# Optimization experiments

Measured on AMD Instinct MI355X. Metric: run time of the kernel, lower is better.

## Reference

```python
import jax, jax.numpy as jnp
import numpy as np

ALPHA = 0.5
TEMP = 0.1
TEMP2 = 0.05  # hardcoded in nt_xent_loss2
NUM_CLASSES = 10
EPS = 1e-12


def setup_inputs() -> dict:
    key = jax.random.key(0)
    k1, k2, k3 = jax.random.split(key, 3)
    B, D, C = 4096, 256, NUM_CLASSES
    cls_feats = jax.random.normal(k1, (B, D), dtype=jnp.float32)
    predicts = jax.random.normal(k2, (B, C), dtype=jnp.float32)
    targets = jax.random.randint(k3, (B,), 0, C)
    return {"cls_feats": cls_feats, "predicts": predicts, "targets": targets}


def _nt_xent_loss(feats, labels):
    B = feats.shape[0]
    eye = jnp.eye(B, dtype=bool)
    same = labels[:, None] == labels[None, :]
    mask = (same & ~eye).astype(feats.dtype)            # positives, no diagonal
    s = jnp.einsum('bd,cd->bc', feats, feats) / TEMP     # [B,B]
    s = jnp.where(eye, 0.0, s)                           # subtract diag_embed(diag)
    logits = s - jax.lax.stop_gradient(jnp.max(s, axis=1, keepdims=True))
    log_denom = jnp.log(jnp.sum(jnp.exp(logits), axis=1, keepdims=True) + EPS)
    log_prob = logits * mask - log_denom
    mask_sum = jnp.sum(mask, axis=1)
    mask_sum = jnp.where(mask_sum == 0, 1.0, mask_sum)
    pos_logits = jnp.sum(mask * log_prob, axis=1) / mask_sum
    return -jnp.mean(pos_logits)


def _nt_xent_loss2(feats, labels):
    B = feats.shape[0]
    eye = jnp.eye(B, dtype=bool)
    same = labels[:, None] == labels[None, :]
    mask = (same & ~eye).astype(feats.dtype)
    diff = ~same                                         # mask2 / different-label pairs
    S = (feats @ feats.T) / TEMP2                        # [B,B]
    val = jnp.where(diff, S, 0.0)                        # dot * different_label_mask

    # The torch loop body depends only on labels[i] -> compute once per class.
    def per_class(c):
        neg = labels != c                                # negatives of class c
        in_sub = neg[:, None] & neg[None, :]             # submatrix membership
        # row max over columns restricted to the negative set
        maxdot = jnp.max(jnp.where(neg[None, :], val, -jnp.inf), axis=1)  # [B]
        shifted = jnp.where(in_sub, val - maxdot[:, None], -jnp.inf)
        s_c = jnp.sum(jnp.exp(shifted))                  # exp_terms.sum()
        n_c = jnp.sum(jnp.where(in_sub, diff, False).astype(jnp.float32))
        return s_c, n_c

    sums, counts = jax.lax.map(jax.checkpoint(per_class), jnp.arange(NUM_CLASSES))
    x = sums[labels]                                     # [B] negtive_dot_negtive_sum
    negsum = counts[labels]                              # [B]
    all_zero = jnp.all(negsum == 0)
    x = jnp.where(all_zero, x, x / negsum)
    log_prob_row = -jnp.log(x + EPS)                     # constant across each row
    mask_sum = jnp.sum(mask, axis=1)
    mask_sum_safe = jnp.where(mask_sum == 0, 1.0, mask_sum)
    pos_logits = (mask_sum * log_prob_row) / mask_sum_safe
    return -jnp.mean(pos_logits)


def reference(cls_feats, predicts, targets):
    norm = jnp.maximum(jnp.linalg.norm(cls_feats, axis=-1, keepdims=True), EPS)
    feats = cls_feats / norm                             # F.normalize(dim=-1)
    logp = jax.nn.log_softmax(predicts, axis=-1)
    ce = -jnp.mean(jnp.take_along_axis(logp, targets[:, None], axis=1)[:, 0])
    cl = _nt_xent_loss(feats, targets)
    tl = _nt_xent_loss2(feats, targets)
    return (1.0 - ALPHA) * ce + ALPHA * cl + 0.5 * ALPHA * tl
```

## Files before the change

kernel.cpp:

```cpp
#include <hip/hip_runtime.h>
#include <math.h>

#define B 4096
#define D 256
#define NC 10
#define LDW 65
#define ZERO4 22528

typedef __attribute__((ext_vector_type(8))) short bf16x8;
typedef __attribute__((ext_vector_type(4))) float f32x4;

__device__ __forceinline__ unsigned short f2bf(float x) {
    unsigned int u = __float_as_uint(x);
    u += 0x7FFFu + ((u >> 16) & 1u);
    return (unsigned short)(u >> 16);
}

__global__ void scatter_kernel(const float* __restrict__ feats, const float* __restrict__ pred,
                               const int* __restrict__ tg, int* __restrict__ labelP,
                               unsigned short* __restrict__ fP, int* __restrict__ h,
                               float* __restrict__ ceP, float4* __restrict__ bigz,
                               float* __restrict__ sums, float* __restrict__ scal,
                               int* __restrict__ done) {
    __shared__ int wcntS[16][NC];
    __shared__ int allS[NC];
    __shared__ int preS[NC];
    __shared__ int cbS[NC];
    __shared__ int posS[256];
    __shared__ float ceS[4];
    const int t = threadIdx.x, w = t >> 6, l = t & 63;
    const int bid = blockIdx.x;
    const int r0 = bid * 256;

    {
        int s0 = bid * 1408 + t;
        bigz[s0] = (float4){0.f, 0.f, 0.f, 0.f};
        if (t < 384) bigz[s0 + 1024] = (float4){0.f, 0.f, 0.f, 0.f};
    }
    if (bid == 0) {
        if (t < 16) sums[t] = 0.f;
        else if (t < 32) scal[t - 16] = 0.f;
        else if (t == 32) *done = 0;
    }

    int4 lv = ((const int4*)tg)[t];
    int labv[4] = {lv.x, lv.y, lv.z, lv.w};
#pragma unroll
    for (int cc = 0; cc < NC; cc++) {
        int cnt = __popcll(__ballot(labv[0] == cc)) + __popcll(__ballot(labv[1] == cc)) +
                  __popcll(__ballot(labv[2] == cc)) + __popcll(__ballot(labv[3] == cc));
        if (l == 0) wcntS[w][cc] = cnt;
    }
    __syncthreads();

    if (t < NC) {
        int all = 0, pre = 0;
#pragma unroll
        for (int ww = 0; ww < 16; ww++) {
            int c = wcntS[ww][t];
            all += c;
            pre += (ww < bid) ? c : 0;
        }
        allS[t] = all;
        preS[t] = pre;
        if (bid == 0) h[t] = all;
    }
    __syncthreads();
    if (t < NC) {
        int b = 0;
#pragma unroll
        for (int cc = 0; cc < NC; cc++) b += (cc < t) ? allS[cc] : 0;
        cbS[t] = b;
    }
    __syncthreads();

    if (w == bid) {
        unsigned long long below = (l == 0) ? 0ull : ((~0ull) >> (64 - l));
        int rnk[4] = {0, 0, 0, 0};
#pragma unroll
        for (int cc = 0; cc < NC; cc++) {
            unsigned long long m0 = __ballot(labv[0] == cc);
            unsigned long long m1 = __ballot(labv[1] == cc);
            unsigned long long m2 = __ballot(labv[2] == cc);
            unsigned long long m3 = __ballot(labv[3] == cc);
            int below4 = __popcll(m0 & below) + __popcll(m1 & below) +
                         __popcll(m2 & below) + __popcll(m3 & below);
#pragma unroll
            for (int e = 0; e < 4; e++)
                if (labv[e] == cc) rnk[e] = below4;
        }
        rnk[1] += (labv[0] == labv[1]);
        rnk[2] += (labv[0] == labv[2]) + (labv[1] == labv[2]);
        rnk[3] += (labv[0] == labv[3]) + (labv[1] == labv[3]) + (labv[2] == labv[3]);
#pragma unroll
        for (int e = 0; e < 4; e++) {
            int c = labv[e];
            int pos = cbS[c] + preS[c] + rnk[e];
            labelP[pos] = c;
            posS[l * 4 + e] = pos;
        }
    }
    if (t < 256) {
        const float* p = pred + (r0 + t) * NC;
        const int c0 = tg[r0 + t];
        float m = p[0];
#pragma unroll
        for (int c = 1; c < NC; c++) m = fmaxf(m, p[c]);
        float s = 0.f;
#pragma unroll
        for (int c = 0; c < NC; c++) s += __expf(p[c] - m);
        float vce = m + logf(s) - p[c0];
#pragma unroll
        for (int o = 1; o < 64; o <<= 1) vce += __shfl_xor(vce, o);
        if (l == 0) ceS[w] = vce;
    }
    __syncthreads();
    if (t == 0) ceP[bid] = ceS[0] + ceS[1] + ceS[2] + ceS[3];

    const int gid = t >> 4, lg = t & 15;
#pragma unroll
    for (int it = 0; it < 4; ++it) {
        const int r = it * 64 + gid;
        float4 v[4];
#pragma unroll
        for (int k = 0; k < 4; k++) v[k] = ((const float4*)feats)[(r0 + r) * 64 + lg * 4 + k];
        float ss = 0.f;
#pragma unroll
        for (int k = 0; k < 4; k++)
            ss += v[k].x * v[k].x + v[k].y * v[k].y + v[k].z * v[k].z + v[k].w * v[k].w;
#pragma unroll
        for (int o = 1; o < 16; o <<= 1) ss += __shfl_xor(ss, o);
        float inv = 1.0f / fmaxf(sqrtf(ss), 1e-12f);
        bf16x8 o0, o1;
#pragma unroll
        for (int k = 0; k < 4; k++) {
            const float* vp = (const float*)&v[k];
            if (k < 2) {
#pragma unroll
                for (int e = 0; e < 4; e++) o0[k * 4 + e] = (short)f2bf(vp[e] * inv);
            } else {
#pragma unroll
                for (int e = 0; e < 4; e++) o1[(k - 2) * 4 + e] = (short)f2bf(vp[e] * inv);
            }
        }
        const int dst = posS[r];
        ((bf16x8*)fP)[dst * 32 + lg * 2 + 0] = o0;
        ((bf16x8*)fP)[dst * 32 + lg * 2 + 1] = o1;
    }
}

__launch_bounds__(256)
__global__ void gemm_kernel(const unsigned short* __restrict__ fP,
                            const int* __restrict__ labP,
                            float* __restrict__ E1, float* __restrict__ P1,
                            float* __restrict__ E2G, int* __restrict__ M2K) {
    __shared__ float scW[4][16 * LDW];
    __shared__ int labS[256];
    __shared__ float E2L[32 * 11];
    __shared__ int M2L[32 * 11];
    __shared__ float E1L[32], P1L[32];

    const int t = threadIdx.x;
    const int w = t >> 6, l = t & 63;
    const int qr = l >> 4, lm = l & 15;
    const int row0 = blockIdx.x * 32;
    const int colB = blockIdx.y * 256;

    labS[t] = labP[colB + t];
    for (int s = t; s < 32 * 11; s += 256) { E2L[s] = 0.f; M2L[s] = 0; }
    if (t < 32) { E1L[t] = 0.f; P1L[t] = 0.f; }

    int liR[2];
#pragma unroll
    for (int mb = 0; mb < 2; mb++) liR[mb] = labP[row0 + mb * 16 + lm];

    const unsigned short* pa = fP + (row0 + lm) * D + qr * 8;
    const unsigned short* pb = fP + (colB + w * 64 + lm) * D + qr * 8;

    f32x4 acc[2][4];
#pragma unroll
    for (int mb = 0; mb < 2; mb++)
#pragma unroll
        for (int nb = 0; nb < 4; nb++) acc[mb][nb] = (f32x4){0.f, 0.f, 0.f, 0.f};

#pragma unroll 2
    for (int ks = 0; ks < 8; ks++) {
        bf16x8 af[2], bfr[4];
#pragma unroll
        for (int mb = 0; mb < 2; mb++) af[mb] = *(const bf16x8*)(pa + mb * 16 * D + ks * 32);
#pragma unroll
        for (int nb = 0; nb < 4; nb++) bfr[nb] = *(const bf16x8*)(pb + nb * 16 * D + ks * 32);
#pragma unroll
        for (int mb = 0; mb < 2; mb++)
#pragma unroll
            for (int nb = 0; nb < 4; nb++)
                acc[mb][nb] = __builtin_amdgcn_mfma_f32_16x16x32_bf16(af[mb], bfr[nb],
                                                                      acc[mb][nb], 0, 0, 0);
    }
    __syncthreads();

#pragma unroll
    for (int mb = 0; mb < 2; mb++) {
#pragma unroll
        for (int nb = 0; nb < 4; nb++)
#pragma unroll
            for (int r = 0; r < 4; r++)
                scW[w][(qr * 4 + r) * LDW + nb * 16 + lm] = acc[mb][nb][r];
        const int rowL = mb * 16 + lm;
        const int li = liR[mb];
        const int rg = row0 + mb * 16 + lm;
        const float* srow = &scW[w][lm * LDW + qr * 16];
        const int colg0 = colB + w * 64 + qr * 16;
        float e1sumA = 0.f, e1sumB = 0.f, p1sum = 0.f;
        int seg = -1; float segEA = 0.f, segEB = 0.f; int segK = 0;
#pragma unroll
        for (int j = 0; j < 16; j++) {
            float g = srow[j];
            int lj = labS[w * 64 + qr * 16 + j];
            bool diag = (colg0 + j == rg);
            float s1 = diag ? 0.f : 10.f * g;
            float e1 = __expf(s1);
            if (j & 1) e1sumB += e1; else e1sumA += e1;
            p1sum += (lj == li && !diag) ? s1 : 0.f;
            if (lj != seg) {
                if (seg >= 0) {
                    atomicAdd(&E2L[rowL * 11 + seg], segEA + segEB);
                    atomicMax(&M2L[rowL * 11 + seg], segK);
                }
                seg = lj; segEA = 0.f; segEB = 0.f; segK = 0;
            }
            if (j & 1) segEB += e1 * e1; else segEA += e1 * e1;
            segK = max(segK, __float_as_int(20.f * g + 64.f));
        }
        atomicAdd(&E2L[rowL * 11 + seg], segEA + segEB);
        atomicMax(&M2L[rowL * 11 + seg], segK);
        float e1sum = e1sumA + e1sumB;
        e1sum += __shfl_xor(e1sum, 16); e1sum += __shfl_xor(e1sum, 32);
        p1sum += __shfl_xor(p1sum, 16); p1sum += __shfl_xor(p1sum, 32);
        if (qr == 0) {
            atomicAdd(&E1L[rowL], e1sum);
            atomicAdd(&P1L[rowL], p1sum);
        }
    }
    __syncthreads();

    if (t < 32) {
        atomicAdd(&E1[row0 + t], E1L[t]);
        atomicAdd(&P1[row0 + t], P1L[t]);
    }
    for (int s = t; s < 32 * NC; s += 256) {
        int r = s / NC, c = s - r * NC;
        float e = E2L[r * 11 + c];
        int k = M2L[r * 11 + c];
        if (e > 0.f) atomicAdd(&E2G[(row0 + r) * NC + c], e);
        if (k > 0) atomicMax(&M2K[(row0 + r) * NC + c], k);
    }
}

__global__ void rowfin_kernel(const int* __restrict__ labP, const int* __restrict__ h,
                              const float* __restrict__ E1, const float* __restrict__ P1,
                              const float* __restrict__ E2G, const int* __restrict__ M2K,
                              const float* __restrict__ ceP, float* __restrict__ sums,
                              float* __restrict__ scal, int* __restrict__ done,
                              float* __restrict__ out) {
    __shared__ float p1S[4];
    __shared__ int lastS;
    const int t = threadIdx.x, w = t >> 6, l = t & 63;
    const int i = blockIdx.x * 256 + t;
    const int li = labP[i];
    float E2[NC], M2[NC];
#pragma unroll
    for (int k = 0; k < NC; k++) {
        E2[k] = E2G[i * NC + k];
        int key = M2K[i * NC + k];
        M2[k] = (key > 0) ? (__int_as_float(key) - 64.f) : -3.0e38f;
    }
    const int hl = h[li];
    E2[li] = (float)hl;
    M2[li] = 0.f;
    float m1 = -3.0e38f, m2 = -3.0e38f;
    int a1 = -1;
#pragma unroll
    for (int k = 0; k < NC; k++) {
        float v = M2[k];
        if (v > m1) { m2 = m1; m1 = v; a1 = k; }
        else if (v > m2) m2 = v;
    }
    float Es = 0.f;
#pragma unroll
    for (int k = 0; k < NC; k++) Es += E2[k];
    float contrib[NC];
#pragma unroll
    for (int c = 0; c < NC; c++) {
        float T = Es - E2[c];
        float md = (a1 == c) ? m2 : m1;
        contrib[c] = (c != li && T > 0.f) ? __expf(-md) * T : 0.f;
    }
#pragma unroll
    for (int c = 0; c < NC; c++) {
        float v = contrib[c];
#pragma unroll
        for (int o = 1; o < 64; o <<= 1) v += __shfl_xor(v, o);
        if (l == 0 && v > 0.f) atomicAdd(&sums[c], v);
    }
    float cn = (float)(hl - 1);
    float pos1 = (cn > 0.f) ? (P1[i] / cn - logf(E1[i])) : 0.f;
#pragma unroll
    for (int o = 1; o < 64; o <<= 1) pos1 += __shfl_xor(pos1, o);
    if (l == 0) p1S[w] = pos1;
    __syncthreads();
    if (t == 0) atomicAdd(&scal[1], p1S[0] + p1S[1] + p1S[2] + p1S[3]);

    __threadfence();
    if (t == 0) lastS = (atomicAdd(done, 1) == 15);
    __syncthreads();
    if (lastS && t == 0) {
        int hh[NC];
        long long S2 = 0;
        for (int c = 0; c < NC; c++) { hh[c] = h[c]; S2 += (long long)hh[c] * hh[c]; }
        float ncs[NC];
        int az = 1;
        for (int c = 0; c < NC; c++) {
            long long M = (long long)B - hh[c];
            long long n = M * M - (S2 - (long long)hh[c] * hh[c]);
            ncs[c] = (float)n;
            if (hh[c] > 0 && n != 0) az = 0;
        }
        float possum = 0.f;
        for (int c = 0; c < NC; c++) {
            if (hh[c] > 1) {
                float x = atomicAdd(&sums[c], 0.f);
                if (!az) x = x / ncs[c];
                possum += (float)hh[c] * (-logf(x + 1e-12f));
            }
        }
        float cesum = 0.f;
        for (int b = 0; b < 16; b++) cesum += ceP[b];
        float ce = cesum / (float)B;
        float cl = -(atomicAdd(&scal[1], 0.f) / (float)B);
        float tl = -(possum / (float)B);
        float loss = 0.5f * ce + 0.5f * cl + 0.25f * tl;
        unsigned int bits = __float_as_uint(loss);
        unsigned int hedged = (bits & 0xFFFF0000u) | (bits >> 16);
        *(unsigned int*)out = hedged;
    }
}

extern "C" void kernel_launch(void* const* d_in, const int* in_sizes, int n_in,
                              void* d_out, int out_size, void* d_ws, size_t ws_size,
                              hipStream_t stream) {
    (void)in_sizes; (void)n_in; (void)out_size; (void)ws_size;
    const float* feats = (const float*)d_in[0];
    const float* pred = (const float*)d_in[1];
    const int* tg = (const int*)d_in[2];
    float* out = (float*)d_out;

    unsigned short* fP = (unsigned short*)d_ws;
    float* E1 = (float*)(fP + B * D);
    float* P1 = E1 + B;
    float* E2G = P1 + B;
    int* M2K = (int*)(E2G + B * NC);
    int* h = M2K + B * NC;
    float* ceP = (float*)(h + 16);
    float* sums = ceP + 16;
    float* scal = sums + 16;
    int* done = (int*)(scal + 16);
    int* labelP = done + 16;

    scatter_kernel<<<B / 256, 1024, 0, stream>>>(feats, pred, tg, labelP, fP, h, ceP,
                                                 (float4*)E1, sums, scal, done);
    gemm_kernel<<<dim3(B / 32, B / 256), 256, 0, stream>>>(fP, labelP, E1, P1, E2G, M2K);
    rowfin_kernel<<<B / 256, 256, 0, stream>>>(labelP, h, E1, P1, E2G, M2K, ceP,
                                               sums, scal, done, out);
}
```

Baseline: 136.5 us.

## Spread scatter/rowfin over more blocks and move diagonal correction out of GEMM epilogue

The scatter kernel goes from 16 blocks of 1024 threads to 64 blocks of 256 threads, and the row-finalize kernel goes from 16×256 to 64×64, so these small phases cover more CUs. The per-element diagonal test in the GEMM epilogue is removed. Instead, each row's bf16 self-dot is computed in scatter and subtracted in rowfin from the exp-sum and the positive-logit sum. This trims epilogue ALU work but adds a D1 buffer and more atomics to the shared accumulators. It also depends on the self-dot computed from bf16 matching the GEMM's diagonal value closely.

```diff
diff --git a/kernel.cpp b/kernel.cpp
--- a/kernel.cpp
+++ b/kernel.cpp
@@ -19,23 +19,19 @@
 __global__ void scatter_kernel(const float* __restrict__ feats, const float* __restrict__ pred,
                                const int* __restrict__ tg, int* __restrict__ labelP,
                                unsigned short* __restrict__ fP, int* __restrict__ h,
-                               float* __restrict__ ceP, float4* __restrict__ bigz,
-                               float* __restrict__ sums, float* __restrict__ scal,
-                               int* __restrict__ done) {
-    __shared__ int wcntS[16][NC];
-    __shared__ int allS[NC];
-    __shared__ int preS[NC];
-    __shared__ int cbS[NC];
-    __shared__ int posS[256];
-    __shared__ float ceS[4];
+                               float* __restrict__ ceP, float* __restrict__ D1,
+                               float4* __restrict__ bigz, float* __restrict__ sums,
+                               float* __restrict__ scal, int* __restrict__ done) {
+    __shared__ int wcntS[4][NC], wpreS[4][NC];
+    __shared__ int allS[NC], preS[NC], cbS[NC];
+    __shared__ int posS[64];
     const int t = threadIdx.x, w = t >> 6, l = t & 63;
-    const int bid = blockIdx.x;
-    const int r0 = bid * 256;
+    const int bid = blockIdx.x, r0 = bid * 64;
 
     {
-        int s0 = bid * 1408 + t;
-        bigz[s0] = (float4){0.f, 0.f, 0.f, 0.f};
-        if (t < 384) bigz[s0 + 1024] = (float4){0.f, 0.f, 0.f, 0.f};
+        int zi = bid * 352 + t;
+        bigz[zi] = (float4){0.f, 0.f, 0.f, 0.f};
+        if (t < 96) bigz[zi + 256] = (float4){0.f, 0.f, 0.f, 0.f};
     }
     if (bid == 0) {
         if (t < 16) sums[t] = 0.f;
@@ -43,24 +39,28 @@
         else if (t == 32) *done = 0;
     }
 
-    int4 lv = ((const int4*)tg)[t];
-    int labv[4] = {lv.x, lv.y, lv.z, lv.w};
-#pragma unroll
-    for (int cc = 0; cc < NC; cc++) {
-        int cnt = __popcll(__ballot(labv[0] == cc)) + __popcll(__ballot(labv[1] == cc)) +
-                  __popcll(__ballot(labv[2] == cc)) + __popcll(__ballot(labv[3] == cc));
-        if (l == 0) wcntS[w][cc] = cnt;
-    }
-    __syncthreads();
-
+    int wc[NC], wp[NC];
+#pragma unroll
+    for (int c = 0; c < NC; c++) { wc[c] = 0; wp[c] = 0; }
+    for (int r = 0; r < 16; ++r) {
+        int lab = tg[w * 1024 + r * 64 + l];
+        bool blw = (w * 16 + r) < bid;
+#pragma unroll
+        for (int c = 0; c < NC; c++) {
+            int p = __popcll(__ballot(lab == c));
+            wc[c] += p;
+            wp[c] += blw ? p : 0;
+        }
+    }
+    if (l == 0) {
+#pragma unroll
+        for (int c = 0; c < NC; c++) { wcntS[w][c] = wc[c]; wpreS[w][c] = wp[c]; }
+    }
+    __syncthreads();
     if (t < NC) {
         int all = 0, pre = 0;
 #pragma unroll
-        for (int ww = 0; ww < 16; ww++) {
-            int c = wcntS[ww][t];
-            all += c;
-            pre += (ww < bid) ? c : 0;
-        }
+        for (int ww = 0; ww < 4; ww++) { all += wcntS[ww][t]; pre += wpreS[ww][t]; }
         allS[t] = all;
         preS[t] = pre;
         if (bid == 0) h[t] = all;
@@ -74,53 +74,36 @@
     }
     __syncthreads();
 
-    if (w == bid) {
-        unsigned long long below = (l == 0) ? 0ull : ((~0ull) >> (64 - l));
-        int rnk[4] = {0, 0, 0, 0};
-#pragma unroll
-        for (int cc = 0; cc < NC; cc++) {
-            unsigned long long m0 = __ballot(labv[0] == cc);
-            unsigned long long m1 = __ballot(labv[1] == cc);
-            unsigned long long m2 = __ballot(labv[2] == cc);
-            unsigned long long m3 = __ballot(labv[3] == cc);
-            int below4 = __popcll(m0 & below) + __popcll(m1 & below) +
-                         __popcll(m2 & below) + __popcll(m3 & below);
-#pragma unroll
-            for (int e = 0; e < 4; e++)
-                if (labv[e] == cc) rnk[e] = below4;
-        }
-        rnk[1] += (labv[0] == labv[1]);
-        rnk[2] += (labv[0] == labv[2]) + (labv[1] == labv[2]);
-        rnk[3] += (labv[0] == labv[3]) + (labv[1] == labv[3]) + (labv[2] == labv[3]);
-#pragma unroll
-        for (int e = 0; e < 4; e++) {
-            int c = labv[e];
-            int pos = cbS[c] + preS[c] + rnk[e];
-            labelP[pos] = c;
-            posS[l * 4 + e] = pos;
-        }
-    }
-    if (t < 256) {
+    if (t < 64) {
+        const int lab0 = tg[r0 + t];
+        unsigned long long below = (t == 0) ? 0ull : ((~0ull) >> (64 - t));
+        int rank = 0;
+#pragma unroll
+        for (int c = 0; c < NC; c++) {
+            unsigned long long m = __ballot(lab0 == c);
+            if (lab0 == c) rank = __popcll(m & below);
+        }
+        int pos = cbS[lab0] + preS[lab0] + rank;
+        labelP[pos] = lab0;
+        posS[t] = pos;
         const float* p = pred + (r0 + t) * NC;
-        const int c0 = tg[r0 + t];
         float m = p[0];
 #pragma unroll
         for (int c = 1; c < NC; c++) m = fmaxf(m, p[c]);
         float s = 0.f;
 #pragma unroll
         for (int c = 0; c < NC; c++) s += __expf(p[c] - m);
-        float vce = m + logf(s) - p[c0];
+        float vce = m + logf(s) - p[lab0];
 #pragma unroll
         for (int o = 1; o < 64; o <<= 1) vce += __shfl_xor(vce, o);
-        if (l == 0) ceS[w] = vce;
-    }
-    __syncthreads();
-    if (t == 0) ceP[bid] = ceS[0] + ceS[1] + ceS[2] + ceS[3];
+        if (t == 0) ceP[bid] = vce;
+    }
+    __syncthreads();
 
     const int gid = t >> 4, lg = t & 15;
 #pragma unroll
     for (int it = 0; it < 4; ++it) {
-        const int r = it * 64 + gid;
+        const int r = it * 16 + gid;
         float4 v[4];
 #pragma unroll
         for (int k = 0; k < 4; k++) v[k] = ((const float4*)feats)[(r0 + r) * 64 + lg * 4 + k];
@@ -143,9 +126,19 @@
                 for (int e = 0; e < 4; e++) o1[(k - 2) * 4 + e] = (short)f2bf(vp[e] * inv);
             }
         }
+        float gss = 0.f;
+#pragma unroll
+        for (int e = 0; e < 8; e++) {
+            float f0 = __uint_as_float(((unsigned)(unsigned short)o0[e]) << 16);
+            float f1 = __uint_as_float(((unsigned)(unsigned short)o1[e]) << 16);
+            gss += f0 * f0 + f1 * f1;
+        }
+#pragma unroll
+        for (int o = 1; o < 16; o <<= 1) gss += __shfl_xor(gss, o);
         const int dst = posS[r];
         ((bf16x8*)fP)[dst * 32 + lg * 2 + 0] = o0;
         ((bf16x8*)fP)[dst * 32 + lg * 2 + 1] = o1;
+        if (lg == 0) D1[dst] = gss;
     }
 }
 
@@ -208,20 +201,17 @@
                 scW[w][(qr * 4 + r) * LDW + nb * 16 + lm] = acc[mb][nb][r];
         const int rowL = mb * 16 + lm;
         const int li = liR[mb];
-        const int rg = row0 + mb * 16 + lm;
         const float* srow = &scW[w][lm * LDW + qr * 16];
-        const int colg0 = colB + w * 64 + qr * 16;
         float e1sumA = 0.f, e1sumB = 0.f, p1sum = 0.f;
         int seg = -1; float segEA = 0.f, segEB = 0.f; int segK = 0;
 #pragma unroll
         for (int j = 0; j < 16; j++) {
             float g = srow[j];
             int lj = labS[w * 64 + qr * 16 + j];
-            bool diag = (colg0 + j == rg);
-            float s1 = diag ? 0.f : 10.f * g;
-            float e1 = __expf(s1);
+            float g10 = 10.f * g;
+            float e1 = __expf(g10);
             if (j & 1) e1sumB += e1; else e1sumA += e1;
-            p1sum += (lj == li && !diag) ? s1 : 0.f;
+            p1sum += (lj == li) ? g : 0.f;
             if (lj != seg) {
                 if (seg >= 0) {
                     atomicAdd(&E2L[rowL * 11 + seg], segEA + segEB);
@@ -229,8 +219,9 @@
                 }
                 seg = lj; segEA = 0.f; segEB = 0.f; segK = 0;
             }
-            if (j & 1) segEB += e1 * e1; else segEA += e1 * e1;
-            segK = max(segK, __float_as_int(20.f * g + 64.f));
+            float e2 = e1 * e1;
+            if (j & 1) segEB += e2; else segEA += e2;
+            segK = max(segK, __float_as_int(fmaf(2.f, g10, 64.f)));
         }
         atomicAdd(&E2L[rowL * 11 + seg], segEA + segEB);
         atomicMax(&M2L[rowL * 11 + seg], segK);
@@ -239,7 +230,7 @@
         p1sum += __shfl_xor(p1sum, 16); p1sum += __shfl_xor(p1sum, 32);
         if (qr == 0) {
             atomicAdd(&E1L[rowL], e1sum);
-            atomicAdd(&P1L[rowL], p1sum);
+            atomicAdd(&P1L[rowL], p1sum * 10.f);
         }
     }
     __syncthreads();
@@ -260,13 +251,12 @@
 __global__ void rowfin_kernel(const int* __restrict__ labP, const int* __restrict__ h,
                               const float* __restrict__ E1, const float* __restrict__ P1,
                               const float* __restrict__ E2G, const int* __restrict__ M2K,
-                              const float* __restrict__ ceP, float* __restrict__ sums,
-                              float* __restrict__ scal, int* __restrict__ done,
-                              float* __restrict__ out) {
-    __shared__ float p1S[4];
+                              const float* __restrict__ ceP, const float* __restrict__ D1,
+                              float* __restrict__ sums, float* __restrict__ scal,
+                              int* __restrict__ done, float* __restrict__ out) {
     __shared__ int lastS;
-    const int t = threadIdx.x, w = t >> 6, l = t & 63;
-    const int i = blockIdx.x * 256 + t;
+    const int t = threadIdx.x;
+    const int i = blockIdx.x * 64 + t;
     const int li = labP[i];
     float E2[NC], M2[NC];
 #pragma unroll
@@ -301,18 +291,19 @@
         float v = contrib[c];
 #pragma unroll
         for (int o = 1; o < 64; o <<= 1) v += __shfl_xor(v, o);
-        if (l == 0 && v > 0.f) atomicAdd(&sums[c], v);
-    }
+        if (t == 0 && v > 0.f) atomicAdd(&sums[c], v);
+    }
+    const float gii = D1[i];
+    const float E1v = E1[i] + 1.f - __expf(10.f * gii);
+    const float P1v = P1[i] - 10.f * gii;
     float cn = (float)(hl - 1);
-    float pos1 = (cn > 0.f) ? (P1[i] / cn - logf(E1[i])) : 0.f;
+    float pos1 = (cn > 0.f) ? (P1v / cn - logf(E1v)) : 0.f;
 #pragma unroll
     for (int o = 1; o < 64; o <<= 1) pos1 += __shfl_xor(pos1, o);
-    if (l == 0) p1S[w] = pos1;
-    __syncthreads();
-    if (t == 0) atomicAdd(&scal[1], p1S[0] + p1S[1] + p1S[2] + p1S[3]);
+    if (t == 0) atomicAdd(&scal[1], pos1);
 
     __threadfence();
-    if (t == 0) lastS = (atomicAdd(done, 1) == 15);
+    if (t == 0) lastS = (atomicAdd(done, 1) == 63);
     __syncthreads();
     if (lastS && t == 0) {
         int hh[NC];
@@ -335,7 +326,7 @@
             }
         }
         float cesum = 0.f;
-        for (int b = 0; b < 16; b++) cesum += ceP[b];
+        for (int b = 0; b < 64; b++) cesum += ceP[b];
         float ce = cesum / (float)B;
         float cl = -(atomicAdd(&scal[1], 0.f) / (float)B);
         float tl = -(possum / (float)B);
@@ -362,14 +353,15 @@
     int* M2K = (int*)(E2G + B * NC);
     int* h = M2K + B * NC;
     float* ceP = (float*)(h + 16);
-    float* sums = ceP + 16;
+    float* sums = ceP + 64;
     float* scal = sums + 16;
     int* done = (int*)(scal + 16);
     int* labelP = done + 16;
-
-    scatter_kernel<<<B / 256, 1024, 0, stream>>>(feats, pred, tg, labelP, fP, h, ceP,
-                                                 (float4*)E1, sums, scal, done);
+    float* D1 = (float*)(labelP + B);
+
+    scatter_kernel<<<64, 256, 0, stream>>>(feats, pred, tg, labelP, fP, h, ceP, D1,
+                                           (float4*)E1, sums, scal, done);
     gemm_kernel<<<dim3(B / 32, B / 256), 256, 0, stream>>>(fP, labelP, E1, P1, E2G, M2K);
-    rowfin_kernel<<<B / 256, 256, 0, stream>>>(labelP, h, E1, P1, E2G, M2K, ceP,
-                                               sums, scal, done, out);
-}
+    rowfin_kernel<<<64, 64, 0, stream>>>(labelP, h, E1, P1, E2G, M2K, ceP, D1,
+                                         sums, scal, done, out);
+}
```

Measured after the change: 135.4 us, median of 2. About the same (-0.8%).
